# Performance work log

Measured on AMD Instinct MI355X. Metric: run time of the kernel, lower is better.

## Reference

```python
import jax, jax.numpy as jnp
import numpy as np

V, D, G, E, B, S = 50000, 300, 256, 1600000, 64, 64


def setup_inputs() -> dict:
    key = jax.random.key(0)
    k = jax.random.split(key, 6)
    emb = jax.random.normal(k[0], (V, D), jnp.float32) * 0.02
    emb = emb.at[0].set(0.0)  # padding_idx=0
    W1 = jax.random.normal(k[1], (D, G), jnp.float32) * (1.0 / np.sqrt(D))
    b1 = jnp.zeros((G,), jnp.float32)
    W2 = jax.random.normal(k[2], (G, G), jnp.float32) * (1.0 / np.sqrt(G))
    b2 = jnp.zeros((G,), jnp.float32)
    edge_index = jax.random.randint(k[3], (2, E), 0, V, dtype=jnp.int64)
    word_ids = jax.random.randint(k[4], (B, S), 0, V, dtype=jnp.int64)
    return {"emb": emb, "W1": W1, "b1": b1, "W2": W2, "b2": b2,
            "edge_index": edge_index, "word_ids": word_ids}


def _gcn_conv(x, W, b, src, dst, num_nodes):
    """PyG GCNConv: add self-loops, symmetric deg^{-1/2} normalization.
    out_i = sum_{j->i} h_j / sqrt(deg_j * deg_i) + h_i / deg_i + b,
    with deg_i = 1 (self-loop) + in-degree(i), h = x @ W."""
    h = x @ W                                        # (N, G)
    deg = jnp.ones((num_nodes,), h.dtype).at[dst].add(1.0)
    inv_sqrt = jax.lax.rsqrt(deg)                    # (N,)
    coef = inv_sqrt[src] * inv_sqrt[dst]             # (E,)
    agg = jnp.zeros_like(h).at[dst].add(h[src] * coef[:, None])
    agg = agg + h * (inv_sqrt * inv_sqrt)[:, None]   # self-loop term
    return agg + b


def reference(emb, W1, b1, W2, b2, edge_index, word_ids):
    num_nodes = emb.shape[0]
    src, dst = edge_index[0], edge_index[1]
    h = jax.nn.relu(_gcn_conv(emb, W1, b1, src, dst, num_nodes))  # (V, G)
    h = _gcn_conv(h, W2, b2, src, dst, num_nodes)                 # (V, G)
    return h[word_ids]                                            # (B, S, G)
```

## Files before the change

### kernel.cpp

```cpp
#include <hip/hip_runtime.h>
#include <hip/hip_bf16.h>

#define NV 50000
#define ND 300
#define NDP 320
#define NG 256
#define NE 1600000
#define NBS 4096
#define NBUCK 196
#define EPB 4096
#define SCAT_BLOCKS 391
#define CPAD 16
#define GEMM1_BLOCKS 782
#define P2_W1 320
#define P2_W2 256
#define P2_EMB 7813
#define HIST_BLOCKS 1024

typedef short short8 __attribute__((ext_vector_type(8)));
typedef float f32x4 __attribute__((ext_vector_type(4)));
typedef float f32x2 __attribute__((ext_vector_type(2)));
typedef _Float16 half4 __attribute__((ext_vector_type(4)));

__device__ __forceinline__ ushort f2bf(float f) {
    unsigned u = __builtin_bit_cast(unsigned, f);
    unsigned r = (u + 0x7fffu + ((u >> 16) & 1u)) >> 16;
    return (ushort)r;
}
__device__ __forceinline__ float bf2f(ushort h) {
    unsigned u = ((unsigned)h) << 16;
    return __builtin_bit_cast(float, u);
}

__global__ __launch_bounds__(256) void hist_kernel(const int* __restrict__ dst,
                                                   int* __restrict__ bucket_count) {
    __shared__ int bh[NBUCK];
    int t = threadIdx.x;
    for (int b = t; b < NBUCK; b += 256) bh[b] = 0;
    __syncthreads();
    for (int i = blockIdx.x * 256 + t; i * 4 < NE; i += HIST_BLOCKS * 256) {
        int4 d = *(const int4*)(dst + i * 4);
        atomicAdd(&bh[d.x >> 8], 1);
        atomicAdd(&bh[d.y >> 8], 1);
        atomicAdd(&bh[d.z >> 8], 1);
        atomicAdd(&bh[d.w >> 8], 1);
    }
    __syncthreads();
    for (int b = t; b < NBUCK; b += 256)
        if (bh[b]) atomicAdd(&bucket_count[b * CPAD], bh[b]);
}

__global__ __launch_bounds__(256) void bucket_scan(const int* __restrict__ bucket_count,
                                                   int* __restrict__ bucket_base,
                                                   int* __restrict__ bucket_cursor) {
    __shared__ int s[256];
    int t = threadIdx.x;
    int v = (t < NBUCK) ? bucket_count[t * CPAD] : 0;
    s[t] = v;
    __syncthreads();
    for (int d = 1; d < 256; d <<= 1) {
        int x = (t >= d) ? s[t - d] : 0;
        __syncthreads();
        s[t] += x;
        __syncthreads();
    }
    int excl = s[t] - v;
    if (t < NBUCK) {
        bucket_base[t] = excl;
        bucket_cursor[t * CPAD] = excl;
    }
    if (t == 255) bucket_base[NBUCK] = s[255];
}

__global__ __launch_bounds__(256) void prep2_kernel(const int* __restrict__ ei,
                                                    int* __restrict__ bucket_cursor,
                                                    unsigned* __restrict__ rec,
                                                    const float* __restrict__ W1,
                                                    const float* __restrict__ W2,
                                                    ushort* __restrict__ W1Th,
                                                    ushort* __restrict__ W2Th,
                                                    ushort* __restrict__ W2Tl,
                                                    const float* __restrict__ emb,
                                                    ushort* __restrict__ embB) {
    int t = threadIdx.x;
    if (blockIdx.x < SCAT_BLOCKS) {
        __shared__ int cnt[NBUCK];
        __shared__ int basel[NBUCK];
        int e0 = blockIdx.x * EPB;
        for (int b = t; b < NBUCK; b += 256) cnt[b] = 0;
        __syncthreads();
        for (int q = 0; q < EPB / 1024; ++q) {
            int i4 = e0 + q * 1024 + t * 4;
            if (i4 < NE) {
                int4 d = *(const int4*)(ei + NE + i4);
                atomicAdd(&cnt[d.x >> 8], 1);
                atomicAdd(&cnt[d.y >> 8], 1);
                atomicAdd(&cnt[d.z >> 8], 1);
                atomicAdd(&cnt[d.w >> 8], 1);
            }
        }
        __syncthreads();
        for (int b = t; b < NBUCK; b += 256) {
            int c = cnt[b];
            basel[b] = c ? atomicAdd(&bucket_cursor[b * CPAD], c) : 0;
        }
        __syncthreads();
        for (int b = t; b < NBUCK; b += 256) cnt[b] = 0;
        __syncthreads();
        for (int q = 0; q < EPB / 1024; ++q) {
            int i4 = e0 + q * 1024 + t * 4;
            if (i4 < NE) {
                int4 s = *(const int4*)(ei + i4);
                int4 d = *(const int4*)(ei + NE + i4);
                int b0 = d.x >> 8, b1 = d.y >> 8, b2 = d.z >> 8, b3 = d.w >> 8;
                int r0 = atomicAdd(&cnt[b0], 1);
                rec[basel[b0] + r0] = (unsigned)s.x | ((unsigned)(d.x & 255) << 16);
                int r1 = atomicAdd(&cnt[b1], 1);
                rec[basel[b1] + r1] = (unsigned)s.y | ((unsigned)(d.y & 255) << 16);
                int r2 = atomicAdd(&cnt[b2], 1);
                rec[basel[b2] + r2] = (unsigned)s.z | ((unsigned)(d.z & 255) << 16);
                int r3 = atomicAdd(&cnt[b3], 1);
                rec[basel[b3] + r3] = (unsigned)s.w | ((unsigned)(d.w & 255) << 16);
            }
        }
    } else if (blockIdx.x < SCAT_BLOCKS + P2_W1) {
        int idx = (blockIdx.x - SCAT_BLOCKS) * 256 + t;
        int n = idx / NDP, k = idx - n * NDP;
        float v = (k < ND) ? W1[(size_t)k * NG + n] : 0.f;
        W1Th[idx] = f2bf(v);
    } else if (blockIdx.x < SCAT_BLOCKS + P2_W1 + P2_W2) {
        int j = (blockIdx.x - SCAT_BLOCKS - P2_W1) * 256 + t;
        int n = j / NG, k = j - n * NG;
        float v = W2[(size_t)k * NG + n];
        ushort h = f2bf(v);
        W2Th[j] = h;
        W2Tl[j] = f2bf(v - bf2f(h));
    } else {
        int u = (blockIdx.x - SCAT_BLOCKS - P2_W1 - P2_W2) * 256 + t;
        if (u < NV * 40) {
            int row = u / 40;
            int kq = (u - row * 40) * 8;
            short8 o;
            if (kq + 8 <= ND) {
                float4 p0 = *(const float4*)(emb + (size_t)row * ND + kq);
                float4 p1 = *(const float4*)(emb + (size_t)row * ND + kq + 4);
                o[0] = (short)f2bf(p0.x); o[1] = (short)f2bf(p0.y);
                o[2] = (short)f2bf(p0.z); o[3] = (short)f2bf(p0.w);
                o[4] = (short)f2bf(p1.x); o[5] = (short)f2bf(p1.y);
                o[6] = (short)f2bf(p1.z); o[7] = (short)f2bf(p1.w);
            } else {
#pragma unroll
                for (int e = 0; e < 8; ++e) {
                    int k = kq + e;
                    float v = (k < ND) ? emb[(size_t)row * ND + k] : 0.f;
                    o[e] = (short)f2bf(v);
                }
            }
            *(short8*)(embB + (size_t)row * NDP + kq) = o;
        }
    }
}

__global__ __launch_bounds__(256) void csr_gemm1(const unsigned* __restrict__ rec,
                                                 const int* __restrict__ bucket_base,
                                                 int* __restrict__ off,
                                                 float* __restrict__ inv_sqrt,
                                                 ushort* __restrict__ csr_src,
                                                 const ushort* __restrict__ embB,
                                                 const ushort* __restrict__ BTh,
                                                 unsigned char* __restrict__ C8) {
    int t = threadIdx.x;
    if (blockIdx.x < NBUCK) {
        __shared__ int degl[256];
        __shared__ int s[256];
        int b = blockIdx.x;
        degl[t] = 0;
        __syncthreads();
        int r0 = bucket_base[b], r1 = bucket_base[b + 1];
        for (int i = r0 + t; i < r1; i += 256)
            atomicAdd(&degl[(rec[i] >> 16) & 255], 1);
        __syncthreads();
        int v = degl[t];
        s[t] = v;
        __syncthreads();
        for (int d = 1; d < 256; d <<= 1) {
            int x = (t >= d) ? s[t - d] : 0;
            __syncthreads();
            s[t] += x;
            __syncthreads();
        }
        int excl = s[t] - v + r0;
        int n = (b << 8) + t;
        if (n < NV) {
            off[n] = excl;
            inv_sqrt[n] = rsqrtf((float)(v + 1));
        }
        if (b == NBUCK - 1 && t == 0) off[NV] = NE;
        __syncthreads();
        degl[t] = excl;
        __syncthreads();
        for (int i = r0 + t; i < r1; i += 256) {
            unsigned e = rec[i];
            int p = atomicAdd(&degl[(e >> 16) & 255], 1);
            csr_src[p] = (ushort)(e & 0xffff);
        }
    } else {
        __shared__ short Ah[128][40];
        __shared__ short Bh[128][40];
        const int M = NV, KP = NDP;
        int bid = blockIdx.x - NBUCK;
        int bm = (bid >> 1) * 128;
        int bn = (bid & 1) * 128;
        int lane = t & 63, wv = t >> 6;
        int wm = (wv >> 1) * 64, wn = (wv & 1) * 64;
        int srow = t >> 1;
        int skq = (t & 1) * 16;
        f32x4 acc[4][4];
#pragma unroll
        for (int mi = 0; mi < 4; ++mi)
#pragma unroll
            for (int ni = 0; ni < 4; ++ni) acc[mi][ni] = (f32x4)0.0f;

        for (int k0 = 0; k0 < KP; k0 += 32) {
            int gk = k0 + skq;
            {
                int gr = bm + srow;
                short8 va0, va1;
                if (gr < M) {
                    va0 = *(const short8*)(embB + (size_t)gr * NDP + gk);
                    va1 = *(const short8*)(embB + (size_t)gr * NDP + gk + 8);
                } else {
                    va0 = (short8)0;
                    va1 = (short8)0;
                }
                *(short8*)&Ah[srow][skq] = va0;
                *(short8*)&Ah[srow][skq + 8] = va1;
            }
            {
                int nr = bn + srow;
                short8 bh0 = *(const short8*)(BTh + (size_t)nr * NDP + gk);
                short8 bh1 = *(const short8*)(BTh + (size_t)nr * NDP + gk + 8);
                *(short8*)&Bh[srow][skq] = bh0;
                *(short8*)&Bh[srow][skq + 8] = bh1;
            }
            __syncthreads();
            int m16 = lane & 15, kb = (lane >> 4) * 8;
            short8 a_h[4], b_h[4];
#pragma unroll
            for (int mi = 0; mi < 4; ++mi)
                a_h[mi] = *(const short8*)&Ah[wm + mi * 16 + m16][kb];
#pragma unroll
            for (int ni = 0; ni < 4; ++ni)
                b_h[ni] = *(const short8*)&Bh[wn + ni * 16 + m16][kb];
#pragma unroll
            for (int mi = 0; mi < 4; ++mi)
#pragma unroll
                for (int ni = 0; ni < 4; ++ni)
                    acc[mi][ni] = __builtin_amdgcn_mfma_f32_16x16x32_bf16(a_h[mi], b_h[ni], acc[mi][ni], 0, 0, 0);
            __syncthreads();
        }
        int m16 = lane & 15, rq = lane >> 4;
#pragma unroll
        for (int mi = 0; mi < 4; ++mi)
#pragma unroll
            for (int ni = 0; ni < 4; ++ni) {
                int row0 = bm + wm + mi * 16 + rq * 4;
                int col = bn + wn + ni * 16 + m16;
                int p01 = __builtin_amdgcn_cvt_pk_fp8_f32(acc[mi][ni][0], acc[mi][ni][1], 0, false);
                int p23 = __builtin_amdgcn_cvt_pk_fp8_f32(acc[mi][ni][2], acc[mi][ni][3], 0, false);
                if (row0 + 0 < M) C8[(size_t)(row0 + 0) * NG + col] = (unsigned char)(p01 & 0xff);
                if (row0 + 1 < M) C8[(size_t)(row0 + 1) * NG + col] = (unsigned char)((p01 >> 8) & 0xff);
                if (row0 + 2 < M) C8[(size_t)(row0 + 2) * NG + col] = (unsigned char)(p23 & 0xff);
                if (row0 + 3 < M) C8[(size_t)(row0 + 3) * NG + col] = (unsigned char)((p23 >> 8) & 0xff);
            }
    }
}

__global__ __launch_bounds__(256) void gemm_out(const float* __restrict__ A,
                                                int lda,
                                                const ushort* __restrict__ BTh,
                                                const ushort* __restrict__ BTl,
                                                int ldb,
                                                int M, int K, int KP,
                                                float* __restrict__ C32,
                                                const float* __restrict__ bias) {
    __shared__ short Ah[128][40];
    __shared__ short Bh[128][40];
    __shared__ short Bl[128][40];
    int t = threadIdx.x;
    int bm = blockIdx.x * 128;
    int bn = blockIdx.y * 128;
    int lane = t & 63, wv = t >> 6;
    int wm = (wv >> 1) * 64, wn = (wv & 1) * 64;
    int srow = t >> 1;
    int skq = (t & 1) * 16;
    f32x4 acc[4][4];
#pragma unroll
    for (int mi = 0; mi < 4; ++mi)
#pragma unroll
        for (int ni = 0; ni < 4; ++ni) acc[mi][ni] = (f32x4)0.0f;

    for (int k0 = 0; k0 < KP; k0 += 32) {
        int gk = k0 + skq;
        {
            int gr = bm + srow;
            short va[16];
            float v[16];
            if (gr < M && gk < K) {
#pragma unroll
                for (int q = 0; q < 4; ++q) {
                    float4 p = *(const float4*)(A + (size_t)gr * lda + gk + q * 4);
                    v[q * 4 + 0] = p.x; v[q * 4 + 1] = p.y;
                    v[q * 4 + 2] = p.z; v[q * 4 + 3] = p.w;
                }
            } else {
#pragma unroll
                for (int e = 0; e < 16; ++e) v[e] = 0.f;
            }
#pragma unroll
            for (int e = 0; e < 16; ++e) va[e] = (short)f2bf(v[e]);
            *(short8*)&Ah[srow][skq] = *(short8*)&va[0];
            *(short8*)&Ah[srow][skq + 8] = *(short8*)&va[8];
        }
        {
            int nr = bn + srow;
            short8 bh0 = *(const short8*)(BTh + (size_t)nr * ldb + gk);
            short8 bh1 = *(const short8*)(BTh + (size_t)nr * ldb + gk + 8);
            short8 bl0 = *(const short8*)(BTl + (size_t)nr * ldb + gk);
            short8 bl1 = *(const short8*)(BTl + (size_t)nr * ldb + gk + 8);
            *(short8*)&Bh[srow][skq] = bh0;
            *(short8*)&Bh[srow][skq + 8] = bh1;
            *(short8*)&Bl[srow][skq] = bl0;
            *(short8*)&Bl[srow][skq + 8] = bl1;
        }
        __syncthreads();
        int m16 = lane & 15, kb = (lane >> 4) * 8;
        short8 a_h[4], b_h[4], b_l[4];
#pragma unroll
        for (int mi = 0; mi < 4; ++mi)
            a_h[mi] = *(const short8*)&Ah[wm + mi * 16 + m16][kb];
#pragma unroll
        for (int ni = 0; ni < 4; ++ni) {
            b_h[ni] = *(const short8*)&Bh[wn + ni * 16 + m16][kb];
            b_l[ni] = *(const short8*)&Bl[wn + ni * 16 + m16][kb];
        }
#pragma unroll
        for (int mi = 0; mi < 4; ++mi)
#pragma unroll
            for (int ni = 0; ni < 4; ++ni) {
                acc[mi][ni] = __builtin_amdgcn_mfma_f32_16x16x32_bf16(a_h[mi], b_h[ni], acc[mi][ni], 0, 0, 0);
                acc[mi][ni] = __builtin_amdgcn_mfma_f32_16x16x32_bf16(a_h[mi], b_l[ni], acc[mi][ni], 0, 0, 0);
            }
        __syncthreads();
    }
    int m16 = lane & 15, rq = lane >> 4;
#pragma unroll
    for (int mi = 0; mi < 4; ++mi)
#pragma unroll
        for (int ni = 0; ni < 4; ++ni) {
#pragma unroll
            for (int r = 0; r < 4; ++r) {
                int row = bm + wm + mi * 16 + rq * 4 + r;
                int col = bn + wn + ni * 16 + m16;
                if (row < M)
                    C32[(size_t)row * NG + col] = acc[mi][ni][r] + bias[col];
            }
        }
}

__global__ __launch_bounds__(256) void agg1_kernel(const unsigned char* __restrict__ h1f8,
                                                   const int* __restrict__ off,
                                                   const ushort* __restrict__ csr_src,
                                                   const float* __restrict__ inv_sqrt,
                                                   const float* __restrict__ b1,
                                                   _Float16* __restrict__ x1) {
    int wv = threadIdx.x >> 6, lane = threadIdx.x & 63;
    int i = blockIdx.x * 4 + wv;
    if (i >= NV) return;
    int c4 = lane * 4;
    int s0 = off[i], s1 = off[i + 1];
    float a0 = 0.f, a1 = 0.f, a2 = 0.f, a3 = 0.f;
    int j = s0;
    for (; j + 16 <= s1; j += 16) {
        int sx[16];
        float wx[16];
        unsigned pk[16];
#pragma unroll
        for (int u = 0; u < 16; ++u) sx[u] = csr_src[j + u];
#pragma unroll
        for (int u = 0; u < 16; ++u) {
            wx[u] = inv_sqrt[sx[u]];
            pk[u] = *(const unsigned*)(h1f8 + (size_t)sx[u] * NG + c4);
        }
#pragma unroll
        for (int u = 0; u < 16; ++u) {
            f32x2 v01 = __builtin_amdgcn_cvt_pk_f32_fp8(pk[u], false);
            f32x2 v23 = __builtin_amdgcn_cvt_pk_f32_fp8(pk[u], true);
            a0 += wx[u] * v01[0];
            a1 += wx[u] * v01[1];
            a2 += wx[u] * v23[0];
            a3 += wx[u] * v23[1];
        }
    }
    for (; j + 4 <= s1; j += 4) {
        int sx[4];
        float wx[4];
        unsigned pk[4];
#pragma unroll
        for (int u = 0; u < 4; ++u) sx[u] = csr_src[j + u];
#pragma unroll
        for (int u = 0; u < 4; ++u) {
            wx[u] = inv_sqrt[sx[u]];
            pk[u] = *(const unsigned*)(h1f8 + (size_t)sx[u] * NG + c4);
        }
#pragma unroll
        for (int u = 0; u < 4; ++u) {
            f32x2 v01 = __builtin_amdgcn_cvt_pk_f32_fp8(pk[u], false);
            f32x2 v23 = __builtin_amdgcn_cvt_pk_f32_fp8(pk[u], true);
            a0 += wx[u] * v01[0];
            a1 += wx[u] * v01[1];
            a2 += wx[u] * v23[0];
            a3 += wx[u] * v23[1];
        }
    }
    for (; j < s1; ++j) {
        int s = csr_src[j];
        float w = inv_sqrt[s];
        unsigned pk = *(const unsigned*)(h1f8 + (size_t)s * NG + c4);
        f32x2 v01 = __builtin_amdgcn_cvt_pk_f32_fp8(pk, false);
        f32x2 v23 = __builtin_amdgcn_cvt_pk_f32_fp8(pk, true);
        a0 += w * v01[0];
        a1 += w * v01[1];
        a2 += w * v23[0];
        a3 += w * v23[1];
    }
    float is = inv_sqrt[i], is2 = is * is;
    unsigned pks = *(const unsigned*)(h1f8 + (size_t)i * NG + c4);
    f32x2 s01 = __builtin_amdgcn_cvt_pk_f32_fp8(pks, false);
    f32x2 s23 = __builtin_amdgcn_cvt_pk_f32_fp8(pks, true);
    float4 bb = *(const float4*)(b1 + c4);
    half4 o;
    o[0] = (_Float16)fmaxf(is * a0 + s01[0] * is2 + bb.x, 0.f);
    o[1] = (_Float16)fmaxf(is * a1 + s01[1] * is2 + bb.y, 0.f);
    o[2] = (_Float16)fmaxf(is * a2 + s23[0] * is2 + bb.z, 0.f);
    o[3] = (_Float16)fmaxf(is * a3 + s23[1] * is2 + bb.w, 0.f);
    *(half4*)(x1 + (size_t)i * NG + c4) = o;
}

__global__ __launch_bounds__(256) void agg2_kernel(const _Float16* __restrict__ x1,
                                                   const int* __restrict__ off,
                                                   const ushort* __restrict__ csr_src,
                                                   const float* __restrict__ inv_sqrt,
                                                   const int* __restrict__ word_ids,
                                                   float* __restrict__ y) {
    int wv = threadIdx.x >> 6, lane = threadIdx.x & 63;
    int p = blockIdx.x * 4 + wv;
    if (p >= NBS) return;
    int n = word_ids[p];
    int c4 = lane * 4;
    int s0 = off[n], s1 = off[n + 1];
    float a0 = 0.f, a1 = 0.f, a2 = 0.f, a3 = 0.f;
    int j = s0;
    for (; j + 16 <= s1; j += 16) {
        int sx[16];
        float wx[16];
        half4 vx[16];
#pragma unroll
        for (int u = 0; u < 16; ++u) sx[u] = csr_src[j + u];
#pragma unroll
        for (int u = 0; u < 16; ++u) {
            wx[u] = inv_sqrt[sx[u]];
            vx[u] = *(const half4*)(x1 + (size_t)sx[u] * NG + c4);
        }
#pragma unroll
        for (int u = 0; u < 16; ++u) {
            a0 += wx[u] * (float)vx[u][0];
            a1 += wx[u] * (float)vx[u][1];
            a2 += wx[u] * (float)vx[u][2];
            a3 += wx[u] * (float)vx[u][3];
        }
    }
    for (; j + 4 <= s1; j += 4) {
        int sx[4];
        float wx[4];
        half4 vx[4];
#pragma unroll
        for (int u = 0; u < 4; ++u) sx[u] = csr_src[j + u];
#pragma unroll
        for (int u = 0; u < 4; ++u) {
            wx[u] = inv_sqrt[sx[u]];
            vx[u] = *(const half4*)(x1 + (size_t)sx[u] * NG + c4);
        }
#pragma unroll
        for (int u = 0; u < 4; ++u) {
            a0 += wx[u] * (float)vx[u][0];
            a1 += wx[u] * (float)vx[u][1];
            a2 += wx[u] * (float)vx[u][2];
            a3 += wx[u] * (float)vx[u][3];
        }
    }
    for (; j < s1; ++j) {
        int s = csr_src[j];
        float w = inv_sqrt[s];
        half4 hv = *(const half4*)(x1 + (size_t)s * NG + c4);
        a0 += w * (float)hv[0];
        a1 += w * (float)hv[1];
        a2 += w * (float)hv[2];
        a3 += w * (float)hv[3];
    }
    float is = inv_sqrt[n], is2 = is * is;
    half4 sv = *(const half4*)(x1 + (size_t)n * NG + c4);
    float4 o;
    o.x = is * a0 + (float)sv[0] * is2;
    o.y = is * a1 + (float)sv[1] * is2;
    o.z = is * a2 + (float)sv[2] * is2;
    o.w = is * a3 + (float)sv[3] * is2;
    *(float4*)(y + (size_t)p * NG + c4) = o;
}

extern "C" void kernel_launch(void* const* d_in, const int* in_sizes, int n_in,
                              void* d_out, int out_size, void* d_ws, size_t ws_size,
                              hipStream_t stream) {
    const float* emb = (const float*)d_in[0];
    const float* W1  = (const float*)d_in[1];
    const float* b1  = (const float*)d_in[2];
    const float* W2  = (const float*)d_in[3];
    const float* b2  = (const float*)d_in[4];
    const int*   ei  = (const int*)d_in[5];
    const int*   wid = (const int*)d_in[6];
    float* out = (float*)d_out;

    char* w = (char*)d_ws;
    auto alloc = [&](size_t bytes) {
        void* p = (void*)w;
        w += (bytes + 255) & ~(size_t)255;
        return p;
    };
    int*    off      = (int*)alloc((size_t)(NV + 1) * 4);
    float*  inv_sqrt = (float*)alloc((size_t)NV * 4);
    int*    bucket_count  = (int*)alloc((size_t)NBUCK * CPAD * 4);
    int*    bucket_base   = (int*)alloc((size_t)(NBUCK + 1) * 4);
    int*    bucket_cursor = (int*)alloc((size_t)NBUCK * CPAD * 4);
    ushort* csr_src  = (ushort*)alloc((size_t)NE * 2);
    unsigned* bucket_rec = (unsigned*)alloc((size_t)NE * 4);
    ushort* W1T_h    = (ushort*)alloc((size_t)NG * NDP * 2);
    ushort* W2T_h    = (ushort*)alloc((size_t)NG * NG * 2);
    ushort* W2T_l    = (ushort*)alloc((size_t)NG * NG * 2);
    ushort* embB     = (ushort*)alloc((size_t)NV * NDP * 2);
    unsigned char* h1f8 = (unsigned char*)alloc((size_t)NV * NG);
    _Float16* x1     = (_Float16*)alloc((size_t)NV * NG * 2);
    float*  y        = (float*)alloc((size_t)NBS * NG * 4);

    hipMemsetAsync(bucket_count, 0, (size_t)NBUCK * CPAD * 4, stream);

    hist_kernel<<<HIST_BLOCKS, 256, 0, stream>>>(ei + NE, bucket_count);
    bucket_scan<<<1, 256, 0, stream>>>(bucket_count, bucket_base, bucket_cursor);
    prep2_kernel<<<SCAT_BLOCKS + P2_W1 + P2_W2 + P2_EMB, 256, 0, stream>>>(
        ei, bucket_cursor, bucket_rec, W1, W2, W1T_h, W2T_h, W2T_l, emb, embB);
    csr_gemm1<<<NBUCK + GEMM1_BLOCKS, 256, 0, stream>>>(bucket_rec, bucket_base,
                                                        off, inv_sqrt, csr_src,
                                                        embB, W1T_h, h1f8);
    agg1_kernel<<<(NV + 3) / 4, 256, 0, stream>>>(h1f8, off, csr_src, inv_sqrt, b1, x1);
    agg2_kernel<<<(NBS + 3) / 4, 256, 0, stream>>>(x1, off, csr_src, inv_sqrt, wid, y);
    {
        dim3 grid((NBS + 127) / 128, NG / 128);
        gemm_out<<<grid, 256, 0, stream>>>(y, NG, W2T_h, W2T_l, NG,
                                           NBS, NG, NG, out, b2);
    }
}
```

Measured before the change: 186.6 us.

## Split fp8 hidden features into 64-column slabs and slice aggregation by column quarter

The GEMM1 epilogue now writes the fp8 hidden matrix as four column-slab arrays of 64 bytes per node instead of 256-byte rows. Layer-1 aggregation launches a 2D grid, one column quarter per y-block. Within each quarter, the 64 lanes split into four groups of 16 that each take every fourth edge, and a shuffle reduction combines the groups. The goal is a smaller per-pass gather footprint that fits cache better and more edge-level parallelism. The cost is four times more index and weight loads, plus scattered byte stores in the GEMM epilogue.

```diff
diff --git a/kernel.cpp b/kernel.cpp
--- a/kernel.cpp
+++ b/kernel.cpp
@@ -168,7 +168,7 @@
                                                  ushort* __restrict__ csr_src,
                                                  const ushort* __restrict__ embB,
                                                  const ushort* __restrict__ BTh,
-                                                 unsigned char* __restrict__ C8) {
+                                                 unsigned char* __restrict__ h1q) {
     int t = threadIdx.x;
     if (blockIdx.x < NBUCK) {
         __shared__ int degl[256];
@@ -266,12 +266,13 @@
             for (int ni = 0; ni < 4; ++ni) {
                 int row0 = bm + wm + mi * 16 + rq * 4;
                 int col = bn + wn + ni * 16 + m16;
+                size_t base = (size_t)(col >> 6) * NV * 64 + (col & 63);
                 int p01 = __builtin_amdgcn_cvt_pk_fp8_f32(acc[mi][ni][0], acc[mi][ni][1], 0, false);
                 int p23 = __builtin_amdgcn_cvt_pk_fp8_f32(acc[mi][ni][2], acc[mi][ni][3], 0, false);
-                if (row0 + 0 < M) C8[(size_t)(row0 + 0) * NG + col] = (unsigned char)(p01 & 0xff);
-                if (row0 + 1 < M) C8[(size_t)(row0 + 1) * NG + col] = (unsigned char)((p01 >> 8) & 0xff);
-                if (row0 + 2 < M) C8[(size_t)(row0 + 2) * NG + col] = (unsigned char)(p23 & 0xff);
-                if (row0 + 3 < M) C8[(size_t)(row0 + 3) * NG + col] = (unsigned char)((p23 >> 8) & 0xff);
+                if (row0 + 0 < M) h1q[base + (size_t)(row0 + 0) * 64] = (unsigned char)(p01 & 0xff);
+                if (row0 + 1 < M) h1q[base + (size_t)(row0 + 1) * 64] = (unsigned char)((p01 >> 8) & 0xff);
+                if (row0 + 2 < M) h1q[base + (size_t)(row0 + 2) * 64] = (unsigned char)(p23 & 0xff);
+                if (row0 + 3 < M) h1q[base + (size_t)(row0 + 3) * 64] = (unsigned char)((p23 >> 8) & 0xff);
             }
     }
 }
@@ -368,7 +369,7 @@
         }
 }
 
-__global__ __launch_bounds__(256) void agg1_kernel(const unsigned char* __restrict__ h1f8,
+__global__ __launch_bounds__(256) void agg1_kernel(const unsigned char* __restrict__ h1q,
                                                    const int* __restrict__ off,
                                                    const ushort* __restrict__ csr_src,
                                                    const float* __restrict__ inv_sqrt,
@@ -377,23 +378,25 @@
     int wv = threadIdx.x >> 6, lane = threadIdx.x & 63;
     int i = blockIdx.x * 4 + wv;
     if (i >= NV) return;
-    int c4 = lane * 4;
+    int q = blockIdx.y;
+    int g = lane >> 4, p = lane & 15;
+    const unsigned char* hb = h1q + (size_t)q * NV * 64;
     int s0 = off[i], s1 = off[i + 1];
     float a0 = 0.f, a1 = 0.f, a2 = 0.f, a3 = 0.f;
     int j = s0;
-    for (; j + 16 <= s1; j += 16) {
-        int sx[16];
-        float wx[16];
-        unsigned pk[16];
-#pragma unroll
-        for (int u = 0; u < 16; ++u) sx[u] = csr_src[j + u];
-#pragma unroll
-        for (int u = 0; u < 16; ++u) {
+    for (; j + 32 <= s1; j += 32) {
+        int sx[8];
+        float wx[8];
+        unsigned pk[8];
+#pragma unroll
+        for (int u = 0; u < 8; ++u) sx[u] = csr_src[j + u * 4 + g];
+#pragma unroll
+        for (int u = 0; u < 8; ++u) {
             wx[u] = inv_sqrt[sx[u]];
-            pk[u] = *(const unsigned*)(h1f8 + (size_t)sx[u] * NG + c4);
-        }
-#pragma unroll
-        for (int u = 0; u < 16; ++u) {
+            pk[u] = *(const unsigned*)(hb + (size_t)sx[u] * 64 + p * 4);
+        }
+#pragma unroll
+        for (int u = 0; u < 8; ++u) {
             f32x2 v01 = __builtin_amdgcn_cvt_pk_f32_fp8(pk[u], false);
             f32x2 v23 = __builtin_amdgcn_cvt_pk_f32_fp8(pk[u], true);
             a0 += wx[u] * v01[0];
@@ -402,31 +405,12 @@
             a3 += wx[u] * v23[1];
         }
     }
-    for (; j + 4 <= s1; j += 4) {
-        int sx[4];
-        float wx[4];
-        unsigned pk[4];
-#pragma unroll
-        for (int u = 0; u < 4; ++u) sx[u] = csr_src[j + u];
-#pragma unroll
-        for (int u = 0; u < 4; ++u) {
-            wx[u] = inv_sqrt[sx[u]];
-            pk[u] = *(const unsigned*)(h1f8 + (size_t)sx[u] * NG + c4);
-        }
-#pragma unroll
-        for (int u = 0; u < 4; ++u) {
-            f32x2 v01 = __builtin_amdgcn_cvt_pk_f32_fp8(pk[u], false);
-            f32x2 v23 = __builtin_amdgcn_cvt_pk_f32_fp8(pk[u], true);
-            a0 += wx[u] * v01[0];
-            a1 += wx[u] * v01[1];
-            a2 += wx[u] * v23[0];
-            a3 += wx[u] * v23[1];
-        }
-    }
-    for (; j < s1; ++j) {
-        int s = csr_src[j];
-        float w = inv_sqrt[s];
-        unsigned pk = *(const unsigned*)(h1f8 + (size_t)s * NG + c4);
+    for (; j < s1; j += 4) {
+        int idx = j + g;
+        bool vld = idx < s1;
+        int sx = csr_src[vld ? idx : s0];
+        float w = vld ? inv_sqrt[sx] : 0.f;
+        unsigned pk = *(const unsigned*)(hb + (size_t)sx * 64 + p * 4);
         f32x2 v01 = __builtin_amdgcn_cvt_pk_f32_fp8(pk, false);
         f32x2 v23 = __builtin_amdgcn_cvt_pk_f32_fp8(pk, true);
         a0 += w * v01[0];
@@ -434,17 +418,27 @@
         a2 += w * v23[0];
         a3 += w * v23[1];
     }
-    float is = inv_sqrt[i], is2 = is * is;
-    unsigned pks = *(const unsigned*)(h1f8 + (size_t)i * NG + c4);
-    f32x2 s01 = __builtin_amdgcn_cvt_pk_f32_fp8(pks, false);
-    f32x2 s23 = __builtin_amdgcn_cvt_pk_f32_fp8(pks, true);
-    float4 bb = *(const float4*)(b1 + c4);
-    half4 o;
-    o[0] = (_Float16)fmaxf(is * a0 + s01[0] * is2 + bb.x, 0.f);
-    o[1] = (_Float16)fmaxf(is * a1 + s01[1] * is2 + bb.y, 0.f);
-    o[2] = (_Float16)fmaxf(is * a2 + s23[0] * is2 + bb.z, 0.f);
-    o[3] = (_Float16)fmaxf(is * a3 + s23[1] * is2 + bb.w, 0.f);
-    *(half4*)(x1 + (size_t)i * NG + c4) = o;
+    a0 += __shfl_xor(a0, 16, 64);
+    a1 += __shfl_xor(a1, 16, 64);
+    a2 += __shfl_xor(a2, 16, 64);
+    a3 += __shfl_xor(a3, 16, 64);
+    a0 += __shfl_xor(a0, 32, 64);
+    a1 += __shfl_xor(a1, 32, 64);
+    a2 += __shfl_xor(a2, 32, 64);
+    a3 += __shfl_xor(a3, 32, 64);
+    if (g == 0) {
+        float is = inv_sqrt[i], is2 = is * is;
+        unsigned pks = *(const unsigned*)(hb + (size_t)i * 64 + p * 4);
+        f32x2 s01 = __builtin_amdgcn_cvt_pk_f32_fp8(pks, false);
+        f32x2 s23 = __builtin_amdgcn_cvt_pk_f32_fp8(pks, true);
+        float4 bb = *(const float4*)(b1 + q * 64 + p * 4);
+        half4 o;
+        o[0] = (_Float16)fmaxf(is * a0 + s01[0] * is2 + bb.x, 0.f);
+        o[1] = (_Float16)fmaxf(is * a1 + s01[1] * is2 + bb.y, 0.f);
+        o[2] = (_Float16)fmaxf(is * a2 + s23[0] * is2 + bb.z, 0.f);
+        o[3] = (_Float16)fmaxf(is * a3 + s23[1] * is2 + bb.w, 0.f);
+        *(half4*)(x1 + (size_t)i * NG + q * 64 + p * 4) = o;
+    }
 }
 
 __global__ __launch_bounds__(256) void agg2_kernel(const _Float16* __restrict__ x1,
@@ -547,7 +541,7 @@
     ushort* W2T_h    = (ushort*)alloc((size_t)NG * NG * 2);
     ushort* W2T_l    = (ushort*)alloc((size_t)NG * NG * 2);
     ushort* embB     = (ushort*)alloc((size_t)NV * NDP * 2);
-    unsigned char* h1f8 = (unsigned char*)alloc((size_t)NV * NG);
+    unsigned char* h1q = (unsigned char*)alloc((size_t)NV * NG);
     _Float16* x1     = (_Float16*)alloc((size_t)NV * NG * 2);
     float*  y        = (float*)alloc((size_t)NBS * NG * 4);
 
@@ -559,8 +553,11 @@
         ei, bucket_cursor, bucket_rec, W1, W2, W1T_h, W2T_h, W2T_l, emb, embB);
     csr_gemm1<<<NBUCK + GEMM1_BLOCKS, 256, 0, stream>>>(bucket_rec, bucket_base,
                                                         off, inv_sqrt, csr_src,
-                                                        embB, W1T_h, h1f8);
-    agg1_kernel<<<(NV + 3) / 4, 256, 0, stream>>>(h1f8, off, csr_src, inv_sqrt, b1, x1);
+                                                        embB, W1T_h, h1q);
+    {
+        dim3 grid((NV + 3) / 4, 4);
+        agg1_kernel<<<grid, 256, 0, stream>>>(h1q, off, csr_src, inv_sqrt, b1, x1);
+    }
     agg2_kernel<<<(NBS + 3) / 4, 256, 0, stream>>>(x1, off, csr_src, inv_sqrt, wid, y);
     {
         dim3 grid((NBS + 127) / 128, NG / 128);
```

Measured after the change: 266.8 us. +43.0%, slower.
